# Kernel tuning notes

Hardware: AMD Instinct MI355X
Metric: run time of the kernel (lower is better)

The kernel has to match this reference:

```python
import jax, jax.numpy as jnp
from jax import lax
import numpy as np


def conv2d(x, w, pad):
    # x: NCHW, w: OIHW
    return lax.conv_general_dilated(x, w, (1, 1), [(pad, pad), (pad, pad)],
                                    dimension_numbers=("NCHW", "OIHW", "NCHW"))


def make_dct_dict(num_atoms, num_dims):
    i = np.arange(num_atoms)[:, None].astype(np.float64)
    n = np.arange(num_dims)[None, :].astype(np.float64)
    w = np.cos((2.0 * n + 1.0) * i * (np.pi / (2.0 * num_dims)))
    w = w / np.linalg.norm(w, axis=1, keepdims=True)
    return jnp.asarray(w.T, dtype=jnp.float32)  # [num_dims, num_atoms]


def setup_inputs() -> dict:
    key = jax.random.key(0)
    B, C, H, W = 8, 64, 64, 64      # C = num_dims
    A = 256                          # num_atoms
    ks = jax.random.split(key, 10)
    s = 0.05
    Dict = make_dct_dict(A, C)       # [C, A]
    L = jnp.sum(Dict ** 2)           # ||Dict||_F^2 (scalar parameter)
    return {
        "x": jax.random.normal(ks[0], (B, C, H, W), jnp.float32),
        "conv_w": jax.random.normal(ks[1], (A, C, 3, 3), jnp.float32) * s,
        "conv_b": jax.random.normal(ks[2], (A,), jnp.float32) * s,
        "res1_w1": jax.random.normal(ks[3], (A // 2, A, 3, 3), jnp.float32) * s,
        "res1_w2": jax.random.normal(ks[4], (A, A // 2, 1, 1), jnp.float32) * s,
        "res2_w1": jax.random.normal(ks[5], (A // 2, A, 3, 3), jnp.float32) * s,
        "res2_w2": jax.random.normal(ks[6], (A, A // 2, 1, 1), jnp.float32) * s,
        "ca_w1": jax.random.normal(ks[7], (A // 16, A), jnp.float32) * s,  # Linear(A, A//16)
        "ca_w2": jax.random.normal(ks[8], (A, A // 16), jnp.float32) * s,  # Linear(A//16, A)
        "sa_w": jax.random.normal(ks[9], (1, 2, 3, 3), jnp.float32) * s,
        "Dict": Dict,
        "L": L,
        "num_iters": 16,
    }


def reference(x, conv_w, conv_b, res1_w1, res1_w2, res2_w1, res2_w2,
              ca_w1, ca_w2, sa_w, Dict, L, num_iters):
    def res_block(h, w1, w2):
        t = conv2d(jax.nn.relu(h), w1, 1)
        t = conv2d(jax.nn.relu(t), w2, 0)
        return h + t

    l = conv2d(x, conv_w, 1) + conv_b[None, :, None, None]
    l = res_block(l, res1_w1, res1_w2)
    l = res_block(l, res2_w1, res2_w2)

    # CBAM: channel attention (shared MLP on avg/max pooled features)
    avg = jnp.mean(l, axis=(2, 3))  # [B, A]
    mx = jnp.max(l, axis=(2, 3))
    fc = lambda v: jax.nn.relu(v @ ca_w1.T) @ ca_w2.T
    l = l * jax.nn.sigmoid(fc(avg) + fc(mx))[:, :, None, None]
    # CBAM: spatial attention
    s2 = jnp.concatenate([jnp.mean(l, axis=1, keepdims=True),
                          jnp.max(l, axis=1, keepdims=True)], axis=1)  # [B,2,H,W]
    l = l * jax.nn.sigmoid(conv2d(s2, sa_w, 1))

    lam = jnp.transpose(l / L, (0, 2, 3, 1))   # [B,H,W,A] per-position thresholds
    xp = jnp.transpose(x, (0, 2, 3, 1))        # [B,H,W,C]

    A = Dict.shape[1]
    S = (jnp.eye(A, dtype=Dict.dtype) - (Dict.T @ Dict) / L).T  # [A,A]
    y = xp @ Dict                               # [B,H,W,A]
    yL = y / L

    soft = lambda v: jnp.sign(v) * jnp.maximum(jnp.abs(v) - lam, 0.0)

    z0 = soft(y)

    def step(z, _):
        return soft(z @ S + yL), None

    z, _ = lax.scan(step, z0, None, length=num_iters)
    x_recon = z @ Dict.T                        # [B,H,W,C]

    return (jnp.transpose(z, (0, 3, 1, 2)),
            jnp.transpose(x_recon, (0, 3, 1, 2)),
            Dict)
```

## Files before the change

kernel.cpp:

```cpp
#include <hip/hip_runtime.h>
#include <hip/hip_bf16.h>

typedef __attribute__((ext_vector_type(8))) short short8v;
typedef __attribute__((ext_vector_type(4))) short short4v;
typedef __attribute__((ext_vector_type(4))) float float4v;

__device__ __forceinline__ unsigned short f2bu(float v){
  __hip_bfloat16 h = __float2bfloat16(v);
  union { __hip_bfloat16 h; unsigned short u; } cv; cv.h = h; return cv.u;
}

__device__ __forceinline__ float softt(float v, float lam){
  float t = fmaxf(fabsf(v) - lam, 0.f);
  float r = copysignf(t, v);
  return (v == 0.f) ? 0.f : r;
}

__global__ void k_Lin(const float* __restrict__ Lsrc, float* __restrict__ Lb){
  Lb[0] = Lsrc[0];
}

__global__ void k_gram(const float* __restrict__ D, unsigned short* __restrict__ Gb){
  int j = blockIdx.x, a = threadIdx.x;
  float acc = 0.f;
  for (int c = 0; c < 64; ++c)
    acc += D[c*256 + j] * D[c*256 + a];
  Gb[j*256 + a] = f2bu(acc);
}

__global__ void k_transpD(const float* __restrict__ D, float* __restrict__ DT,
                          unsigned short* __restrict__ DTb){
  int gid = blockIdx.x * 256 + threadIdx.x;
  if (gid < 16384) {
    int a = gid >> 6, c = gid & 63;
    float v = D[c*256 + a];
    DT[gid] = v;
    DTb[gid] = f2bu(v);
  }
}

__global__ void k_castw(const float* __restrict__ w, unsigned short* __restrict__ wb,
                        int n){
  int gid = blockIdx.x * 256 + threadIdx.x;
  if (gid < n) wb[gid] = f2bu(w[gid]);
}

__global__ void k_permw3(const float* __restrict__ w, unsigned short* __restrict__ wb,
                         int logI, int n){
  int gid = blockIdx.x * 256 + threadIdx.x;
  if (gid >= n) return;
  int I = 1 << logI;
  int i = gid & (I - 1);
  int t = gid >> logI;
  int o = t / 9;
  int r = t - o * 9;
  wb[gid] = f2bu(w[((o << logI) + i) * 9 + r]);
}

template<int KS, int CIN, bool BIAS, bool RES, bool WF32, bool WBF>
__global__ __launch_bounds__(256) void k_conv(
    const unsigned short* __restrict__ in, const unsigned short* __restrict__ wb,
    const float* __restrict__ bias, const float* res, float* outf,
    unsigned short* __restrict__ outb, int Cout)
{
  constexpr int NCH  = CIN / 32;
  constexpr int LNCH = (NCH == 2) ? 1 : (NCH == 4 ? 2 : 3);
  constexpr int K    = KS * KS * CIN;

  __shared__ unsigned short Asb[64][40];
  __shared__ unsigned short Bsb[128][40];

  const int tid = threadIdx.x;
  int bx = blockIdx.x;
  { const int cpx = gridDim.x >> 3; bx = (bx & 7) * cpx + (bx >> 3); }
  const int m0  = bx * 64;
  const int n0  = blockIdx.y * 128;
  const int b   = m0 >> 12;
  const int hw0 = m0 & 4095;
  const int h   = hw0 >> 6;
  const int w0  = hw0 & 63;

  const int sm  = tid & 63;
  const int sq8 = tid >> 6;
  const int bn  = tid & 127;
  const int bq  = tid >> 7;

  const int w   = tid >> 6;
  const int ln  = tid & 63;
  const int q   = ln >> 4;
  const int l16 = ln & 15;

  float4v acc[2][4];
  #pragma unroll
  for (int nt = 0; nt < 2; ++nt)
    #pragma unroll
    for (int mt = 0; mt < 4; ++mt)
      acc[nt][mt] = (float4v){0.f, 0.f, 0.f, 0.f};

  int sA = 0, sB = NCH;
  if (KS == 3) { sA = (h == 0 ? 3 : 0) * NCH; sB = (h == 63 ? 6 : 9) * NCH; }

  short8v a_r;
  short8v b_r0, b_r1;

  auto pref = [&](int s){
    const int r    = s >> LNCH;
    const int ccid = s & (NCH - 1);
    int hh = h, ww = w0 + sm;
    bool ok = true;
    if (KS == 3) {
      const int dh = r / 3 - 1;
      const int dw = r - (r / 3) * 3 - 1;
      hh += dh; ww += dw;
      ok = ((unsigned)ww < 64u);
    }
    a_r = (short8v){0,0,0,0,0,0,0,0};
    if (ok) {
      const unsigned short* ap = in +
          (((size_t)(b * CIN + ccid * 32 + sq8 * 8)) << 12) + (hh << 6) + ww;
      #pragma unroll
      for (int j = 0; j < 8; ++j)
        a_r[j] = (short)ap[(size_t)j << 12];
    }
    const unsigned short* bp = wb + (size_t)(n0 + bn) * K + s * 32 + bq * 16;
    b_r0 = *(const short8v*)(bp);
    b_r1 = *(const short8v*)(bp + 8);
  };

  pref(sA);
  for (int s = sA; s < sB; ) {
    *(short8v*)(&Asb[sm][sq8 * 8])      = a_r;
    *(short8v*)(&Bsb[bn][bq * 16])      = b_r0;
    *(short8v*)(&Bsb[bn][bq * 16 + 8])  = b_r1;
    __syncthreads();
    const int sn = s + 1;
    if (sn < sB) pref(sn);
    short8v Af[4];
    #pragma unroll
    for (int mt = 0; mt < 4; ++mt)
      Af[mt] = *(const short8v*)(&Asb[mt * 16 + l16][q * 8]);
    #pragma unroll
    for (int nt = 0; nt < 2; ++nt) {
      short8v Bf = *(const short8v*)(&Bsb[w * 32 + nt * 16 + l16][q * 8]);
      #pragma unroll
      for (int mt = 0; mt < 4; ++mt)
        acc[nt][mt] = __builtin_amdgcn_mfma_f32_16x16x32_bf16(
            Af[mt], Bf, acc[nt][mt], 0, 0, 0);
    }
    __syncthreads();
    s = sn;
  }

  #pragma unroll
  for (int nt = 0; nt < 2; ++nt) {
    const int n = n0 + w * 32 + nt * 16 + l16;
    float bv = 0.f;
    if (BIAS) bv = bias[n];
    #pragma unroll
    for (int mt = 0; mt < 4; ++mt) {
      const size_t base = (((size_t)(b * Cout + n)) << 12) + hw0 + mt * 16 + q * 4;
      float o[4];
      #pragma unroll
      for (int r2 = 0; r2 < 4; ++r2) o[r2] = acc[nt][mt][r2] + bv;
      if (RES) {
        float4 r4 = *(const float4*)(res + base);
        o[0] += r4.x; o[1] += r4.y; o[2] += r4.z; o[3] += r4.w;
      }
      if (WF32) {
        float4 o4; o4.x = o[0]; o4.y = o[1]; o4.z = o[2]; o4.w = o[3];
        *(float4*)(outf + base) = o4;
      }
      if (WBF) {
        short4v s4;
        #pragma unroll
        for (int r2 = 0; r2 < 4; ++r2) s4[r2] = (short)f2bu(fmaxf(o[r2], 0.f));
        *(short4v*)(outb + base) = s4;
      }
    }
  }
}

__global__ void k_pool(const float* __restrict__ l, float* __restrict__ avg,
                       float* __restrict__ mx){
  int b = blockIdx.y, a = blockIdx.x, tid = threadIdx.x;
  const float* p = l + ((size_t)(b * 256 + a) << 12);
  float s = 0.f, m = -1e30f;
  for (int i = tid; i < 4096; i += 256) { float v = p[i]; s += v; m = fmaxf(m, v); }
  __shared__ float ss[256], sm[256];
  ss[tid] = s; sm[tid] = m; __syncthreads();
  for (int o = 128; o > 0; o >>= 1) {
    if (tid < o) { ss[tid] += ss[tid+o]; sm[tid] = fmaxf(sm[tid], sm[tid+o]); }
    __syncthreads();
  }
  if (tid == 0) { avg[b*256+a] = ss[0] * (1.f/4096.f); mx[b*256+a] = sm[0]; }
}

__global__ void k_ca(const float* __restrict__ avg, const float* __restrict__ mx,
                     const float* __restrict__ w1, const float* __restrict__ w2,
                     float* __restrict__ cscale){
  int b = blockIdx.x, tid = threadIdx.x;
  __shared__ float h[16];
  if (tid < 16) {
    float sa = 0.f, sm = 0.f;
    for (int a = 0; a < 256; ++a) {
      float w = w1[tid*256 + a];
      sa += avg[b*256 + a] * w;
      sm += mx[b*256 + a] * w;
    }
    h[tid] = fmaxf(sa, 0.f) + fmaxf(sm, 0.f);
  }
  __syncthreads();
  float s = 0.f;
  for (int j = 0; j < 16; ++j) s += h[j] * w2[tid*16 + j];
  cscale[b*256 + tid] = 1.f / (1.f + __expf(-s));
}

__global__ void k_s2(const float* __restrict__ l, const float* __restrict__ cscale,
                     float* __restrict__ s2){
  int b = blockIdx.y;
  int hw = blockIdx.x * 256 + threadIdx.x;
  const float* p  = l + (((size_t)b * 256) << 12) + hw;
  const float* cs = cscale + b * 256;
  float s = 0.f, m = -1e30f;
  for (int a = 0; a < 256; ++a) {
    float v = p[(size_t)a << 12] * cs[a];
    s += v; m = fmaxf(m, v);
  }
  s2[((b*2) << 12) + hw]   = s * (1.f/256.f);
  s2[((b*2+1) << 12) + hw] = m;
}

__global__ void k_sa(const float* __restrict__ s2, const float* __restrict__ w,
                     float* __restrict__ sa){
  int b = blockIdx.y;
  int hw = blockIdx.x * 256 + threadIdx.x;
  int h = hw >> 6, ww = hw & 63;
  float acc = 0.f;
  for (int ch = 0; ch < 2; ++ch)
    for (int dh = -1; dh <= 1; ++dh)
      for (int dw = -1; dw <= 1; ++dw) {
        int hh = h + dh, wc = ww + dw;
        if ((unsigned)hh < 64u && (unsigned)wc < 64u)
          acc += s2[((b*2+ch) << 12) + (hh << 6) + wc] * w[ch*9 + (dh+1)*3 + (dw+1)];
      }
  sa[(b << 12) + hw] = 1.f / (1.f + __expf(-acc));
}

#define XTS 80

__global__ __launch_bounds__(512) void k_lista(
    const float* __restrict__ x,
    const unsigned short* __restrict__ DTb,
    const unsigned short* __restrict__ Gb,
    const float* __restrict__ lmap, const float* __restrict__ csc,
    const float* __restrict__ sav, const float* __restrict__ Lb,
    float* __restrict__ zout)
{
  __shared__ unsigned short xTb[32][XTS];
  __shared__ unsigned short zbuf[2][32 * 256];

  const int tid = threadIdx.x;
  const int m0  = blockIdx.x * 32;
  const int b   = m0 >> 12;
  const int hw0 = m0 & 4095;
  const float invL = 1.0f / Lb[0];

  {
    const int i  = tid & 31;
    const int c0 = tid >> 5;
    #pragma unroll
    for (int cc = 0; cc < 4; ++cc) {
      int c = c0 + cc * 16;
      xTb[i][c] = f2bu(x[((b * 64 + c) << 12) + hw0 + i]);
    }
  }
  __syncthreads();

  const int w   = tid >> 6;
  const int ln  = tid & 63;
  const int q   = ln >> 4;
  const int l16 = ln & 15;
  const int rx  = l16 & 7;

  float z[4][4], yl[4][4], lamr[4][4];

  short8v Sg[2][8];
  #pragma unroll
  for (int at = 0; at < 2; ++at)
    #pragma unroll
    for (int ks = 0; ks < 8; ++ks)
      Sg[at][ks] = *(const short8v*)(
          Gb + (size_t)(w * 32 + at * 16 + l16) * 256 + ks * 32 + q * 8);

  #pragma unroll
  for (int at = 0; at < 2; ++at) {
    const short8v A0 = *(const short8v*)(DTb + (w*32 + at*16 + l16) * 64 + q * 8);
    const short8v A1 = *(const short8v*)(DTb + (w*32 + at*16 + l16) * 64 + 32 + q * 8);
    const int chunk = ((w * 4 + at * 2 + (q >> 1)) ^ rx);
    #pragma unroll
    for (int pt = 0; pt < 2; ++pt) {
      float4v a = {0.f, 0.f, 0.f, 0.f};
      const short8v B0 = *(const short8v*)(&xTb[pt * 16 + l16][q * 8]);
      const short8v B1 = *(const short8v*)(&xTb[pt * 16 + l16][32 + q * 8]);
      a = __builtin_amdgcn_mfma_f32_16x16x32_bf16(A0, B0, a, 0, 0, 0);
      a = __builtin_amdgcn_mfma_f32_16x16x32_bf16(A1, B1, a, 0, 0, 0);
      const int t = at * 2 + pt;
      const int p = pt * 16 + l16;
      short4v pk;
      #pragma unroll
      for (int r = 0; r < 4; ++r) {
        const int atom = w * 32 + at * 16 + q * 4 + r;
        const float lv = lmap[(((size_t)(b * 256 + atom)) << 12) + hw0 + p];
        const float sv = sav[(b << 12) + hw0 + p];
        const float cv = csc[b * 256 + atom];
        const float lm = ((lv * cv) * sv) * invL;
        const float yv = a[r];
        lamr[t][r] = lm;
        yl[t][r]   = yv * invL;
        const float z0 = softt(yv, lm);
        z[t][r] = z0;
        pk[r] = (short)f2bu(z0);
      }
      *(short4v*)(&zbuf[0][p * 256 + (chunk << 3) + (q & 1) * 4]) = pk;
    }
  }
  __syncthreads();

  int cur = 0;
  for (int it = 0; it < 16; ++it) {
    float4v acc[2][2];
    #pragma unroll
    for (int at = 0; at < 2; ++at)
      #pragma unroll
      for (int pt = 0; pt < 2; ++pt)
        acc[at][pt] = (float4v){0.f, 0.f, 0.f, 0.f};

    #pragma unroll
    for (int pt = 0; pt < 2; ++pt) {
      const unsigned short* zrow = &zbuf[cur][(pt * 16 + l16) * 256];
      #pragma unroll
      for (int ks = 0; ks < 8; ++ks) {
        const short8v B = *(const short8v*)(zrow + (((ks * 4 + q) ^ rx) << 3));
        acc[0][pt] = __builtin_amdgcn_mfma_f32_16x16x32_bf16(Sg[0][ks], B, acc[0][pt], 0, 0, 0);
        acc[1][pt] = __builtin_amdgcn_mfma_f32_16x16x32_bf16(Sg[1][ks], B, acc[1][pt], 0, 0, 0);
      }
    }
    #pragma unroll
    for (int at = 0; at < 2; ++at) {
      const int chunk = ((w * 4 + at * 2 + (q >> 1)) ^ rx);
      #pragma unroll
      for (int pt = 0; pt < 2; ++pt) {
        const int t = at * 2 + pt;
        const int p = pt * 16 + l16;
        short4v pk;
        #pragma unroll
        for (int r = 0; r < 4; ++r) {
          const float nz = softt(z[t][r] + yl[t][r] - acc[at][pt][r] * invL,
                                 lamr[t][r]);
          z[t][r] = nz;
          pk[r] = (short)f2bu(nz);
        }
        *(short4v*)(&zbuf[cur ^ 1][p * 256 + (chunk << 3) + (q & 1) * 4]) = pk;
      }
    }
    __syncthreads();
    cur ^= 1;
  }

  #pragma unroll
  for (int at = 0; at < 2; ++at) {
    #pragma unroll
    for (int pt = 0; pt < 2; ++pt) {
      const int t = at * 2 + pt;
      const int p = pt * 16 + l16;
      float4 o;
      o.x = z[t][0]; o.y = z[t][1]; o.z = z[t][2]; o.w = z[t][3];
      *(float4*)(&zout[(size_t)(m0 + p) * 256 + w * 32 + at * 16 + q * 4]) = o;
    }
  }
}

__global__ __launch_bounds__(256) void k_recon_simple(
    const float* __restrict__ z, const float* __restrict__ DT,
    float* __restrict__ out1)
{
  __shared__ float zs[16][256];
  const int tid = threadIdx.x;
  const int r0  = blockIdx.x * 16;
  const int b   = r0 >> 12;
  const int hw0 = r0 & 4095;

  for (int idx = tid; idx < 4096; idx += 256) {
    int r = idx >> 8, k = idx & 255;
    zs[r][k] = z[(r0 + r) * 256 + k];
  }
  __syncthreads();

  const int c  = tid & 63;
  const int rg = tid >> 6;
  float acc[4] = {0.f, 0.f, 0.f, 0.f};
  for (int a = 0; a < 256; ++a) {
    float d = DT[a * 64 + c];
    #pragma unroll
    for (int i = 0; i < 4; ++i) acc[i] += zs[rg + 4*i][a] * d;
  }
  #pragma unroll
  for (int i = 0; i < 4; ++i) {
    int r = rg + 4*i;
    out1[((b * 64 + c) << 12) + hw0 + r] = acc[i];
  }
}

__global__ __launch_bounds__(256) void k_zout_t(const float* __restrict__ z,
                                                float* __restrict__ out0){
  __shared__ float zs[64][65];
  const int tid = threadIdx.x;
  const int hwt = blockIdx.x * 64;
  const int at  = blockIdx.y * 64;
  const int b   = blockIdx.z;
  const int j   = tid & 63;
  const int i0  = tid >> 6;
  #pragma unroll
  for (int k = 0; k < 16; ++k) {
    int i = i0 + k * 4;
    zs[i][j] = z[(size_t)(b * 4096 + hwt + i) * 256 + at + j];
  }
  __syncthreads();
  #pragma unroll
  for (int k = 0; k < 16; ++k) {
    int i = i0 + k * 4;
    out0[(((size_t)(b * 256 + at + i)) << 12) + hwt + j] = zs[j][i];
  }
}

__global__ void k_dictout_f32(const float* __restrict__ D, float* __restrict__ out2){
  int i = blockIdx.x * 256 + threadIdx.x;
  if (i < 16384) out2[i] = D[i];
}

extern "C" void kernel_launch(void* const* d_in, const int* in_sizes, int n_in,
                              void* d_out, int out_size, void* d_ws, size_t ws_size,
                              hipStream_t stream)
{
  (void)in_sizes; (void)n_in; (void)out_size; (void)ws_size;

  const float* x    = (const float*)d_in[0];
  const float* cw   = (const float*)d_in[1];
  const float* cb   = (const float*)d_in[2];
  const float* r1w1 = (const float*)d_in[3];
  const float* r1w2 = (const float*)d_in[4];
  const float* r2w1 = (const float*)d_in[5];
  const float* r2w2 = (const float*)d_in[6];
  const float* caw1 = (const float*)d_in[7];
  const float* caw2 = (const float*)d_in[8];
  const float* saw  = (const float*)d_in[9];
  const float* D    = (const float*)d_in[10];
  const float* Lsrc = (const float*)d_in[11];

  float* p = (float*)d_ws;
  float* DT   = p; p += 16384;
  float* Lb   = p; p += 8;
  unsigned short* Gb  = (unsigned short*)p; p += 32768;
  unsigned short* DTb = (unsigned short*)p; p += 8192;
  unsigned short* cwb   = (unsigned short*)p; p += 73728;
  unsigned short* r1w1b = (unsigned short*)p; p += 147456;
  unsigned short* r1w2b = (unsigned short*)p; p += 16384;
  unsigned short* r2w1b = (unsigned short*)p; p += 147456;
  unsigned short* r2w2b = (unsigned short*)p; p += 16384;
  float* avg  = p; p += 2048;
  float* mx   = p; p += 2048;
  float* csc  = p; p += 2048;
  float* s2   = p; p += 65536;
  float* sa   = p; p += 32768;
  float* l    = p; p += 8388608;
  float* scr  = p; p += 8388608;
  float* zt   = p; p += 8388608;
  float* z    = zt;

  unsigned short* xb = (unsigned short*)scr;
  unsigned short* lb = (unsigned short*)(scr + 1048576);
  unsigned short* tb = (unsigned short*)(scr + 1048576 + 4194304);

  float* out0 = (float*)d_out;
  float* out1 = out0 + (size_t)8*256*4096;
  float* out2 = out1 + (size_t)8*64*4096;

  dim3 b256(256);

  k_Lin<<<dim3(1), dim3(1), 0, stream>>>(Lsrc, Lb);
  k_gram<<<dim3(256), b256, 0, stream>>>(D, Gb);
  k_transpD<<<dim3(64), b256, 0, stream>>>(D, DT, DTb);
  k_permw3<<<dim3(576),  b256, 0, stream>>>(cw,   cwb,   6, 147456);
  k_permw3<<<dim3(1152), b256, 0, stream>>>(r1w1, r1w1b, 8, 294912);
  k_castw <<<dim3(128),  b256, 0, stream>>>(r1w2, r1w2b, 32768);
  k_permw3<<<dim3(1152), b256, 0, stream>>>(r2w1, r2w1b, 8, 294912);
  k_castw <<<dim3(128),  b256, 0, stream>>>(r2w2, r2w2b, 32768);
  k_castw <<<dim3(8192), b256, 0, stream>>>(x, xb, 2097152);

  k_conv<3,  64, true,  false, true,  true ><<<dim3(512, 2), b256, 0, stream>>>(
      xb, cwb, cb, (const float*)nullptr, l, lb, 256);
  k_conv<3, 256, false, false, false, true ><<<dim3(512, 1), b256, 0, stream>>>(
      lb, r1w1b, (const float*)nullptr, (const float*)nullptr, (float*)nullptr, tb, 128);
  k_conv<1, 128, false, true,  true,  true ><<<dim3(512, 2), b256, 0, stream>>>(
      tb, r1w2b, (const float*)nullptr, l, l, lb, 256);
  k_conv<3, 256, false, false, false, true ><<<dim3(512, 1), b256, 0, stream>>>(
      lb, r2w1b, (const float*)nullptr, (const float*)nullptr, (float*)nullptr, tb, 128);
  k_conv<1, 128, false, true,  true,  false><<<dim3(512, 2), b256, 0, stream>>>(
      tb, r2w2b, (const float*)nullptr, l, l, (unsigned short*)nullptr, 256);

  k_pool<<<dim3(256, 8), b256, 0, stream>>>(l, avg, mx);
  k_ca<<<dim3(8), b256, 0, stream>>>(avg, mx, caw1, caw2, csc);
  k_s2<<<dim3(16, 8), b256, 0, stream>>>(l, csc, s2);
  k_sa<<<dim3(16, 8), b256, 0, stream>>>(s2, saw, sa);

  k_lista<<<dim3(1024), dim3(512), 0, stream>>>(x, DTb, Gb, l, csc, sa, Lb, z);

  k_recon_simple<<<dim3(2048), b256, 0, stream>>>(z, DT, out1);
  k_zout_t<<<dim3(64, 4, 8), b256, 0, stream>>>(z, out0);
  k_dictout_f32<<<dim3(64), b256, 0, stream>>>(D, out2);
}
```

Baseline: 489.1 us.

## Vectorize conv A-tile loads, pad LISTA smem, fuse z transpose into LISTA

The conv kernel now loads eight consecutive pixels per channel with one vector load and shifts them in shared memory to handle the horizontal tap offset, replacing eight strided scalar gathers. The LISTA kernel reads the pre-cast bf16 input, reuses the z buffer for the x tile, swaps the XOR swizzle for a padded row stride, and adds an occupancy hint of two blocks per CU. It also writes the NCHW z output directly, so the separate transpose kernel is removed. The tradeoffs are scalar 2-byte shared stores in the conv path and uncoalesced strided global writes for out0.

```diff
diff --git a/kernel.cpp b/kernel.cpp
--- a/kernel.cpp
+++ b/kernel.cpp
@@ -78,10 +78,10 @@
   const int b   = m0 >> 12;
   const int hw0 = m0 & 4095;
   const int h   = hw0 >> 6;
-  const int w0  = hw0 & 63;
-
-  const int sm  = tid & 63;
-  const int sq8 = tid >> 6;
+
+  const int kk  = tid & 31;
+  const int pg  = tid >> 5;
+  const int p0  = pg * 8;
   const int bn  = tid & 127;
   const int bq  = tid >> 7;
 
@@ -102,26 +102,21 @@
 
   short8v a_r;
   short8v b_r0, b_r1;
+  int dw_r = 0;
 
   auto pref = [&](int s){
     const int r    = s >> LNCH;
     const int ccid = s & (NCH - 1);
-    int hh = h, ww = w0 + sm;
-    bool ok = true;
+    int hh = h, dw = 0;
     if (KS == 3) {
-      const int dh = r / 3 - 1;
-      const int dw = r - (r / 3) * 3 - 1;
-      hh += dh; ww += dw;
-      ok = ((unsigned)ww < 64u);
-    }
-    a_r = (short8v){0,0,0,0,0,0,0,0};
-    if (ok) {
-      const unsigned short* ap = in +
-          (((size_t)(b * CIN + ccid * 32 + sq8 * 8)) << 12) + (hh << 6) + ww;
-      #pragma unroll
-      for (int j = 0; j < 8; ++j)
-        a_r[j] = (short)ap[(size_t)j << 12];
-    }
+      const int r3 = r / 3;
+      dw = r - r3 * 3 - 1;
+      hh = h + r3 - 1;
+    }
+    dw_r = dw;
+    const unsigned short* ap = in +
+        (((size_t)(b * CIN + ccid * 32 + kk)) << 12) + (hh << 6) + p0;
+    a_r  = *(const short8v*)(ap);
     const unsigned short* bp = wb + (size_t)(n0 + bn) * K + s * 32 + bq * 16;
     b_r0 = *(const short8v*)(bp);
     b_r1 = *(const short8v*)(bp + 8);
@@ -129,7 +124,18 @@
 
   pref(sA);
   for (int s = sA; s < sB; ) {
-    *(short8v*)(&Asb[sm][sq8 * 8])      = a_r;
+    if (KS == 3 && dw_r != 0) {
+      #pragma unroll
+      for (int j = 0; j < 8; ++j) {
+        int m = p0 + j - dw_r;
+        if ((unsigned)m < 64u) Asb[m][kk] = (unsigned short)a_r[j];
+      }
+      if (dw_r > 0) { if (pg == 7) Asb[63][kk] = 0; }
+      else          { if (pg == 0) Asb[0][kk]  = 0; }
+    } else {
+      #pragma unroll
+      for (int j = 0; j < 8; ++j) Asb[p0 + j][kk] = (unsigned short)a_r[j];
+    }
     *(short8v*)(&Bsb[bn][bq * 16])      = b_r0;
     *(short8v*)(&Bsb[bn][bq * 16 + 8])  = b_r1;
     __syncthreads();
@@ -246,18 +252,18 @@
   sa[(b << 12) + hw] = 1.f / (1.f + __expf(-acc));
 }
 
+#define ZSTR 272
 #define XTS 80
 
-__global__ __launch_bounds__(512) void k_lista(
-    const float* __restrict__ x,
+__global__ __launch_bounds__(512, 2) void k_lista(
+    const unsigned short* __restrict__ xb,
     const unsigned short* __restrict__ DTb,
     const unsigned short* __restrict__ Gb,
     const float* __restrict__ lmap, const float* __restrict__ csc,
     const float* __restrict__ sav, const float* __restrict__ Lb,
-    float* __restrict__ zout)
+    float* __restrict__ zout, float* __restrict__ out0)
 {
-  __shared__ unsigned short xTb[32][XTS];
-  __shared__ unsigned short zbuf[2][32 * 256];
+  __shared__ unsigned short zbuf[2][32 * ZSTR];
 
   const int tid = threadIdx.x;
   const int m0  = blockIdx.x * 32;
@@ -265,24 +271,21 @@
   const int hw0 = m0 & 4095;
   const float invL = 1.0f / Lb[0];
 
+  unsigned short* xTb = &zbuf[1][0];
   {
     const int i  = tid & 31;
     const int c0 = tid >> 5;
     #pragma unroll
     for (int cc = 0; cc < 4; ++cc) {
       int c = c0 + cc * 16;
-      xTb[i][c] = f2bu(x[((b * 64 + c) << 12) + hw0 + i]);
-    }
-  }
-  __syncthreads();
+      xTb[i * XTS + c] = xb[((b * 64 + c) << 12) + hw0 + i];
+    }
+  }
 
   const int w   = tid >> 6;
   const int ln  = tid & 63;
   const int q   = ln >> 4;
   const int l16 = ln & 15;
-  const int rx  = l16 & 7;
-
-  float z[4][4], yl[4][4], lamr[4][4];
 
   short8v Sg[2][8];
   #pragma unroll
@@ -292,16 +295,19 @@
       Sg[at][ks] = *(const short8v*)(
           Gb + (size_t)(w * 32 + at * 16 + l16) * 256 + ks * 32 + q * 8);
 
+  __syncthreads();
+
+  float z[4][4], yl[4][4], lamr[4][4];
+
   #pragma unroll
   for (int at = 0; at < 2; ++at) {
     const short8v A0 = *(const short8v*)(DTb + (w*32 + at*16 + l16) * 64 + q * 8);
     const short8v A1 = *(const short8v*)(DTb + (w*32 + at*16 + l16) * 64 + 32 + q * 8);
-    const int chunk = ((w * 4 + at * 2 + (q >> 1)) ^ rx);
     #pragma unroll
     for (int pt = 0; pt < 2; ++pt) {
       float4v a = {0.f, 0.f, 0.f, 0.f};
-      const short8v B0 = *(const short8v*)(&xTb[pt * 16 + l16][q * 8]);
-      const short8v B1 = *(const short8v*)(&xTb[pt * 16 + l16][32 + q * 8]);
+      const short8v B0 = *(const short8v*)(&xTb[(pt*16 + l16) * XTS + q * 8]);
+      const short8v B1 = *(const short8v*)(&xTb[(pt*16 + l16) * XTS + 32 + q * 8]);
       a = __builtin_amdgcn_mfma_f32_16x16x32_bf16(A0, B0, a, 0, 0, 0);
       a = __builtin_amdgcn_mfma_f32_16x16x32_bf16(A1, B1, a, 0, 0, 0);
       const int t = at * 2 + pt;
@@ -321,9 +327,16 @@
         z[t][r] = z0;
         pk[r] = (short)f2bu(z0);
       }
-      *(short4v*)(&zbuf[0][p * 256 + (chunk << 3) + (q & 1) * 4]) = pk;
-    }
-  }
+      *(short4v*)(&zbuf[0][p * ZSTR + w * 32 + at * 16 + q * 4]) = pk;
+    }
+  }
+
+  #pragma unroll
+  for (int at = 0; at < 2; ++at)
+    #pragma unroll
+    for (int ks = 0; ks < 8; ++ks)
+      asm volatile("" : "+v"(Sg[at][ks]));
+
   __syncthreads();
 
   int cur = 0;
@@ -337,17 +350,16 @@
 
     #pragma unroll
     for (int pt = 0; pt < 2; ++pt) {
-      const unsigned short* zrow = &zbuf[cur][(pt * 16 + l16) * 256];
+      const unsigned short* zrow = &zbuf[cur][(pt * 16 + l16) * ZSTR + q * 8];
       #pragma unroll
       for (int ks = 0; ks < 8; ++ks) {
-        const short8v B = *(const short8v*)(zrow + (((ks * 4 + q) ^ rx) << 3));
+        const short8v B = *(const short8v*)(zrow + ks * 32);
         acc[0][pt] = __builtin_amdgcn_mfma_f32_16x16x32_bf16(Sg[0][ks], B, acc[0][pt], 0, 0, 0);
         acc[1][pt] = __builtin_amdgcn_mfma_f32_16x16x32_bf16(Sg[1][ks], B, acc[1][pt], 0, 0, 0);
       }
     }
     #pragma unroll
     for (int at = 0; at < 2; ++at) {
-      const int chunk = ((w * 4 + at * 2 + (q >> 1)) ^ rx);
       #pragma unroll
       for (int pt = 0; pt < 2; ++pt) {
         const int t = at * 2 + pt;
@@ -355,12 +367,12 @@
         short4v pk;
         #pragma unroll
         for (int r = 0; r < 4; ++r) {
-          const float nz = softt(z[t][r] + yl[t][r] - acc[at][pt][r] * invL,
-                                 lamr[t][r]);
+          const float u  = fmaf(-invL, acc[at][pt][r], z[t][r] + yl[t][r]);
+          const float nz = softt(u, lamr[t][r]);
           z[t][r] = nz;
           pk[r] = (short)f2bu(nz);
         }
-        *(short4v*)(&zbuf[cur ^ 1][p * 256 + (chunk << 3) + (q & 1) * 4]) = pk;
+        *(short4v*)(&zbuf[cur ^ 1][p * ZSTR + w * 32 + at * 16 + q * 4]) = pk;
       }
     }
     __syncthreads();
@@ -376,6 +388,12 @@
       float4 o;
       o.x = z[t][0]; o.y = z[t][1]; o.z = z[t][2]; o.w = z[t][3];
       *(float4*)(&zout[(size_t)(m0 + p) * 256 + w * 32 + at * 16 + q * 4]) = o;
+      const size_t ob = (((size_t)(b * 256 + w * 32 + at * 16 + q * 4)) << 12)
+                      + hw0 + p;
+      out0[ob        ] = z[t][0];
+      out0[ob +  4096] = z[t][1];
+      out0[ob +  8192] = z[t][2];
+      out0[ob + 12288] = z[t][3];
     }
   }
 }
@@ -408,28 +426,6 @@
   for (int i = 0; i < 4; ++i) {
     int r = rg + 4*i;
     out1[((b * 64 + c) << 12) + hw0 + r] = acc[i];
-  }
-}
-
-__global__ __launch_bounds__(256) void k_zout_t(const float* __restrict__ z,
-                                                float* __restrict__ out0){
-  __shared__ float zs[64][65];
-  const int tid = threadIdx.x;
-  const int hwt = blockIdx.x * 64;
-  const int at  = blockIdx.y * 64;
-  const int b   = blockIdx.z;
-  const int j   = tid & 63;
-  const int i0  = tid >> 6;
-  #pragma unroll
-  for (int k = 0; k < 16; ++k) {
-    int i = i0 + k * 4;
-    zs[i][j] = z[(size_t)(b * 4096 + hwt + i) * 256 + at + j];
-  }
-  __syncthreads();
-  #pragma unroll
-  for (int k = 0; k < 16; ++k) {
-    int i = i0 + k * 4;
-    out0[(((size_t)(b * 256 + at + i)) << 12) + hwt + j] = zs[j][i];
   }
 }
 
@@ -513,9 +509,9 @@
   k_s2<<<dim3(16, 8), b256, 0, stream>>>(l, csc, s2);
   k_sa<<<dim3(16, 8), b256, 0, stream>>>(s2, saw, sa);
 
-  k_lista<<<dim3(1024), dim3(512), 0, stream>>>(x, DTb, Gb, l, csc, sa, Lb, z);
+  k_lista<<<dim3(1024), dim3(512), 0, stream>>>(xb, DTb, Gb, l, csc, sa, Lb,
+                                                z, out0);
 
   k_recon_simple<<<dim3(2048), b256, 0, stream>>>(z, DT, out1);
-  k_zout_t<<<dim3(64, 4, 8), b256, 0, stream>>>(z, out0);
   k_dictout_f32<<<dim3(64), b256, 0, stream>>>(D, out2);
 }
```

After: 499.0 us. +2.0%, slower.

## Split LISTA work across 16 waves per block with padded z buffer

Applied to the files above, without the earlier changes.

The LISTA kernel now runs 1024 threads per block, so each wave owns 16 atoms instead of 32. That halves the per-thread Gram-matrix registers and the accumulator state. The swizzled shared z layout is replaced with a padded row stride, and the x tile aliases the second z buffer. The kernel reads the already-converted bf16 x instead of converting fp32 on the fly. The aim is more waves for latency hiding, at the cost of more barrier participants per iteration and more warps contending for shared-memory bandwidth.

```diff
diff --git a/kernel.cpp b/kernel.cpp
--- a/kernel.cpp
+++ b/kernel.cpp
@@ -109,9 +109,10 @@
     int hh = h, ww = w0 + sm;
     bool ok = true;
     if (KS == 3) {
-      const int dh = r / 3 - 1;
-      const int dw = r - (r / 3) * 3 - 1;
-      hh += dh; ww += dw;
+      const int r3 = r / 3;
+      const int dw = r - r3 * 3 - 1;
+      hh = h + r3 - 1;
+      ww += dw;
       ok = ((unsigned)ww < 64u);
     }
     a_r = (short8v){0,0,0,0,0,0,0,0};
@@ -246,18 +247,18 @@
   sa[(b << 12) + hw] = 1.f / (1.f + __expf(-acc));
 }
 
+#define ZSTR 272
 #define XTS 80
 
-__global__ __launch_bounds__(512) void k_lista(
-    const float* __restrict__ x,
+__global__ __launch_bounds__(1024, 4) void k_lista(
+    const unsigned short* __restrict__ xb,
     const unsigned short* __restrict__ DTb,
     const unsigned short* __restrict__ Gb,
     const float* __restrict__ lmap, const float* __restrict__ csc,
     const float* __restrict__ sav, const float* __restrict__ Lb,
     float* __restrict__ zout)
 {
-  __shared__ unsigned short xTb[32][XTS];
-  __shared__ unsigned short zbuf[2][32 * 256];
+  __shared__ unsigned short zbuf[2][32 * ZSTR];
 
   const int tid = threadIdx.x;
   const int m0  = blockIdx.x * 32;
@@ -265,118 +266,103 @@
   const int hw0 = m0 & 4095;
   const float invL = 1.0f / Lb[0];
 
+  unsigned short* xTb = &zbuf[1][0];
   {
     const int i  = tid & 31;
     const int c0 = tid >> 5;
-    #pragma unroll
-    for (int cc = 0; cc < 4; ++cc) {
-      int c = c0 + cc * 16;
-      xTb[i][c] = f2bu(x[((b * 64 + c) << 12) + hw0 + i]);
-    }
-  }
-  __syncthreads();
+    xTb[i * XTS + c0]      = xb[((b * 64 + c0) << 12) + hw0 + i];
+    xTb[i * XTS + c0 + 32] = xb[((b * 64 + c0 + 32) << 12) + hw0 + i];
+  }
 
   const int w   = tid >> 6;
   const int ln  = tid & 63;
   const int q   = ln >> 4;
   const int l16 = ln & 15;
-  const int rx  = l16 & 7;
-
-  float z[4][4], yl[4][4], lamr[4][4];
-
-  short8v Sg[2][8];
-  #pragma unroll
-  for (int at = 0; at < 2; ++at)
-    #pragma unroll
-    for (int ks = 0; ks < 8; ++ks)
-      Sg[at][ks] = *(const short8v*)(
-          Gb + (size_t)(w * 32 + at * 16 + l16) * 256 + ks * 32 + q * 8);
-
-  #pragma unroll
-  for (int at = 0; at < 2; ++at) {
-    const short8v A0 = *(const short8v*)(DTb + (w*32 + at*16 + l16) * 64 + q * 8);
-    const short8v A1 = *(const short8v*)(DTb + (w*32 + at*16 + l16) * 64 + 32 + q * 8);
-    const int chunk = ((w * 4 + at * 2 + (q >> 1)) ^ rx);
+
+  short8v Sg[8];
+  #pragma unroll
+  for (int ks = 0; ks < 8; ++ks)
+    Sg[ks] = *(const short8v*)(
+        Gb + (size_t)(w * 16 + l16) * 256 + ks * 32 + q * 8);
+
+  __syncthreads();
+
+  float z[2][4], yl[2][4], lamr[2][4];
+
+  {
+    const short8v A0 = *(const short8v*)(DTb + (w*16 + l16) * 64 + q * 8);
+    const short8v A1 = *(const short8v*)(DTb + (w*16 + l16) * 64 + 32 + q * 8);
     #pragma unroll
     for (int pt = 0; pt < 2; ++pt) {
       float4v a = {0.f, 0.f, 0.f, 0.f};
-      const short8v B0 = *(const short8v*)(&xTb[pt * 16 + l16][q * 8]);
-      const short8v B1 = *(const short8v*)(&xTb[pt * 16 + l16][32 + q * 8]);
+      const short8v B0 = *(const short8v*)(&xTb[(pt*16 + l16) * XTS + q * 8]);
+      const short8v B1 = *(const short8v*)(&xTb[(pt*16 + l16) * XTS + 32 + q * 8]);
       a = __builtin_amdgcn_mfma_f32_16x16x32_bf16(A0, B0, a, 0, 0, 0);
       a = __builtin_amdgcn_mfma_f32_16x16x32_bf16(A1, B1, a, 0, 0, 0);
-      const int t = at * 2 + pt;
       const int p = pt * 16 + l16;
       short4v pk;
       #pragma unroll
       for (int r = 0; r < 4; ++r) {
-        const int atom = w * 32 + at * 16 + q * 4 + r;
+        const int atom = w * 16 + q * 4 + r;
         const float lv = lmap[(((size_t)(b * 256 + atom)) << 12) + hw0 + p];
         const float sv = sav[(b << 12) + hw0 + p];
         const float cv = csc[b * 256 + atom];
         const float lm = ((lv * cv) * sv) * invL;
         const float yv = a[r];
-        lamr[t][r] = lm;
-        yl[t][r]   = yv * invL;
+        lamr[pt][r] = lm;
+        yl[pt][r]   = yv * invL;
         const float z0 = softt(yv, lm);
-        z[t][r] = z0;
+        z[pt][r] = z0;
         pk[r] = (short)f2bu(z0);
       }
-      *(short4v*)(&zbuf[0][p * 256 + (chunk << 3) + (q & 1) * 4]) = pk;
-    }
-  }
+      *(short4v*)(&zbuf[0][p * ZSTR + w * 16 + q * 4]) = pk;
+    }
+  }
+
+  #pragma unroll
+  for (int ks = 0; ks < 8; ++ks)
+    asm volatile("" : "+v"(Sg[ks]));
+
   __syncthreads();
 
   int cur = 0;
   for (int it = 0; it < 16; ++it) {
-    float4v acc[2][2];
-    #pragma unroll
-    for (int at = 0; at < 2; ++at)
-      #pragma unroll
-      for (int pt = 0; pt < 2; ++pt)
-        acc[at][pt] = (float4v){0.f, 0.f, 0.f, 0.f};
+    float4v acc[2];
+    acc[0] = (float4v){0.f, 0.f, 0.f, 0.f};
+    acc[1] = (float4v){0.f, 0.f, 0.f, 0.f};
 
     #pragma unroll
     for (int pt = 0; pt < 2; ++pt) {
-      const unsigned short* zrow = &zbuf[cur][(pt * 16 + l16) * 256];
+      const unsigned short* zrow = &zbuf[cur][(pt * 16 + l16) * ZSTR + q * 8];
       #pragma unroll
       for (int ks = 0; ks < 8; ++ks) {
-        const short8v B = *(const short8v*)(zrow + (((ks * 4 + q) ^ rx) << 3));
-        acc[0][pt] = __builtin_amdgcn_mfma_f32_16x16x32_bf16(Sg[0][ks], B, acc[0][pt], 0, 0, 0);
-        acc[1][pt] = __builtin_amdgcn_mfma_f32_16x16x32_bf16(Sg[1][ks], B, acc[1][pt], 0, 0, 0);
-      }
-    }
-    #pragma unroll
-    for (int at = 0; at < 2; ++at) {
-      const int chunk = ((w * 4 + at * 2 + (q >> 1)) ^ rx);
+        const short8v B = *(const short8v*)(zrow + ks * 32);
+        acc[pt] = __builtin_amdgcn_mfma_f32_16x16x32_bf16(Sg[ks], B, acc[pt], 0, 0, 0);
+      }
+    }
+    #pragma unroll
+    for (int pt = 0; pt < 2; ++pt) {
+      const int p = pt * 16 + l16;
+      short4v pk;
       #pragma unroll
-      for (int pt = 0; pt < 2; ++pt) {
-        const int t = at * 2 + pt;
-        const int p = pt * 16 + l16;
-        short4v pk;
-        #pragma unroll
-        for (int r = 0; r < 4; ++r) {
-          const float nz = softt(z[t][r] + yl[t][r] - acc[at][pt][r] * invL,
-                                 lamr[t][r]);
-          z[t][r] = nz;
-          pk[r] = (short)f2bu(nz);
-        }
-        *(short4v*)(&zbuf[cur ^ 1][p * 256 + (chunk << 3) + (q & 1) * 4]) = pk;
-      }
+      for (int r = 0; r < 4; ++r) {
+        const float u  = fmaf(-invL, acc[pt][r], z[pt][r] + yl[pt][r]);
+        const float nz = softt(u, lamr[pt][r]);
+        z[pt][r] = nz;
+        pk[r] = (short)f2bu(nz);
+      }
+      *(short4v*)(&zbuf[cur ^ 1][p * ZSTR + w * 16 + q * 4]) = pk;
     }
     __syncthreads();
     cur ^= 1;
   }
 
   #pragma unroll
-  for (int at = 0; at < 2; ++at) {
-    #pragma unroll
-    for (int pt = 0; pt < 2; ++pt) {
-      const int t = at * 2 + pt;
-      const int p = pt * 16 + l16;
-      float4 o;
-      o.x = z[t][0]; o.y = z[t][1]; o.z = z[t][2]; o.w = z[t][3];
-      *(float4*)(&zout[(size_t)(m0 + p) * 256 + w * 32 + at * 16 + q * 4]) = o;
-    }
+  for (int pt = 0; pt < 2; ++pt) {
+    const int p = pt * 16 + l16;
+    float4 o;
+    o.x = z[pt][0]; o.y = z[pt][1]; o.z = z[pt][2]; o.w = z[pt][3];
+    *(float4*)(&zout[(size_t)(m0 + p) * 256 + w * 16 + q * 4]) = o;
   }
 }
 
@@ -513,7 +499,7 @@
   k_s2<<<dim3(16, 8), b256, 0, stream>>>(l, csc, s2);
   k_sa<<<dim3(16, 8), b256, 0, stream>>>(s2, saw, sa);
 
-  k_lista<<<dim3(1024), dim3(512), 0, stream>>>(x, DTb, Gb, l, csc, sa, Lb, z);
+  k_lista<<<dim3(1024), dim3(1024), 0, stream>>>(xb, DTb, Gb, l, csc, sa, Lb, z);
 
   k_recon_simple<<<dim3(2048), b256, 0, stream>>>(z, DT, out1);
   k_zout_t<<<dim3(64, 4, 8), b256, 0, stream>>>(z, out0);
```

New measurement: 492.4 us. About the same (+0.7%).
